# Kernel optimization log

Measured on AMD Instinct MI355X. Metric: run time of the kernel, lower is better.

## Reference

```python
import jax, jax.numpy as jnp
import numpy as np

NUM_HEADS = 16
EPS_LN = 1e-5
EPS_NORM = 1e-12


def layernorm(x, g, b):
    mu = jnp.mean(x, axis=-1, keepdims=True)
    var = jnp.mean((x - mu) ** 2, axis=-1, keepdims=True)
    return (x - mu) * jax.lax.rsqrt(var + EPS_LN) * g + b


def l2norm(x):
    n = jnp.sqrt(jnp.sum(x * x, axis=-1, keepdims=True))
    return x / jnp.maximum(n, EPS_NORM)


def setup_inputs() -> dict:
    key = jax.random.key(0)
    ks = jax.random.split(key, 12)
    B, N, C = 8, 1024, 1024
    std = 0.02
    inp = {
        "txt_token": jax.random.normal(ks[0], (B, 1, C), jnp.float32),
        "text_features": jax.random.normal(ks[1], (B, N, C), jnp.float32),
        "text_mask": jax.random.randint(ks[2], (B, N), 0, 2).astype(bool),
        "vis_token": jax.random.normal(ks[3], (B, 1, C), jnp.float32),
        "top_lens": 256,
        # parameters
        "Wqkv": jax.random.normal(ks[4], (C, 3 * C), jnp.float32) * std,
        "bqkv": jnp.zeros((3 * C,), jnp.float32),
        "Wp2": jax.random.normal(ks[5], (C, C), jnp.float32) * std,
        "bp2": jnp.zeros((C,), jnp.float32),
        "ln2_g": jnp.ones((C,), jnp.float32),
        "ln2_b": jnp.zeros((C,), jnp.float32),
        "sim_alpha": jnp.ones((1,), jnp.float32),
        "sim_beta": jnp.zeros((1,), jnp.float32),
        "Wp1": jax.random.normal(ks[6], (C, C), jnp.float32) * std,
        "bp1": jnp.zeros((C,), jnp.float32),
        "ln1_g": jnp.ones((C,), jnp.float32),
        "ln1_b": jnp.zeros((C,), jnp.float32),
    }
    return inp


def reference(txt_token, text_features, text_mask, vis_token, top_lens,
              Wqkv, bqkv, Wp2, bp2, ln2_g, ln2_b,
              sim_alpha, sim_beta, Wp1, bp1, ln1_g, ln1_b):
    B, N, C = text_features.shape
    H = NUM_HEADS
    hd = C // H
    scale = hd ** (-0.5)

    qkv = (text_features @ Wqkv + bqkv).reshape(B, N, 3, H, hd)
    q = qkv[:, :, 0].transpose(0, 2, 1, 3)  # [B,H,N,hd]
    k = qkv[:, :, 1].transpose(0, 2, 1, 3)
    v = qkv[:, :, 2].transpose(0, 2, 1, 3)

    attn = jnp.einsum('bhqd,bhkd->bhqk', q, k) * scale  # [B,H,N,N]
    vals, idx = jax.lax.top_k(attn, top_lens)            # [B,H,N,k]
    p = jax.nn.softmax(vals, axis=-1)

    # scatter topk softmax back into zeros at original key positions
    b_ix = jnp.arange(B)[:, None, None, None]
    h_ix = jnp.arange(H)[None, :, None, None]
    q_ix = jnp.arange(N)[None, None, :, None]
    attn_sp = jnp.zeros_like(attn).at[b_ix, h_ix, q_ix, idx].set(p)

    # mask padded keys, then second softmax (dropout = identity in eval)
    attn_sp = jnp.where(text_mask[:, None, None, :], -jnp.inf, attn_sp)
    attn_w = jax.nn.softmax(attn_sp, axis=-1)

    x = jnp.einsum('bhqk,bhkd->bqhd', attn_w, v).reshape(B, N, C)
    x = x @ Wp2 + bp2
    tf = layernorm(text_features + x, ln2_g, ln2_b)  # [B,N,C]

    # cosine-similarity top-k pooling
    sim = sim_beta + sim_alpha * jnp.einsum('bmc,bnc->bmn', l2norm(vis_token), l2norm(tf))  # [B,1,N]
    sim = jax.nn.sigmoid(jnp.where(text_mask[:, None, :], -jnp.inf, sim))
    _, top_idx = jax.lax.top_k(sim, top_lens)        # [B,1,k]
    top_idx = top_idx[:, 0]                           # [B,k]
    top_vecs = jnp.take_along_axis(tf, top_idx[:, :, None], axis=1)  # [B,k,C]
    pooled = jnp.mean(top_vecs, axis=1, keepdims=True)               # [B,1,C]

    tt = pooled + txt_token
    tt = layernorm(tt @ Wp1 + bp1, ln1_g, ln1_b)
    return tt, tf
```

## Files before the change

kernel.cpp:

```cpp
#include <hip/hip_runtime.h>
#include <stdint.h>

typedef unsigned short u16;
typedef float floatx4 __attribute__((ext_vector_type(4)));
typedef short short8 __attribute__((ext_vector_type(8)));

#define TOPK_ 256

#define AS1(p) ((const __attribute__((address_space(1))) void*)(p))
#define AS3(p) ((__attribute__((address_space(3))) void*)(p))

__device__ __forceinline__ u16 f2bf(float f) {
  unsigned u = __builtin_bit_cast(unsigned, f);
  unsigned r = (u + 0x7FFFu + ((u >> 16) & 1u)) >> 16;
  return (u16)r;
}
__device__ __forceinline__ float bf2f(u16 b) {
  unsigned u = ((unsigned)b) << 16;
  return __builtin_bit_cast(float, u);
}

__device__ __forceinline__ float wave_sum_f32(float x) {
#define DPP_STEP(ctrl, rmask)                                                        \
  {                                                                                  \
    float t_ = __builtin_bit_cast(                                                   \
        float, __builtin_amdgcn_update_dpp(0, __builtin_bit_cast(int, x), ctrl,      \
                                           rmask, 0xf, true));                       \
    x += t_;                                                                         \
  }
  DPP_STEP(0x111, 0xf)
  DPP_STEP(0x112, 0xf)
  DPP_STEP(0x114, 0xf)
  DPP_STEP(0x118, 0xf)
  DPP_STEP(0x142, 0xa)
  DPP_STEP(0x143, 0xc)
#undef DPP_STEP
  return __builtin_bit_cast(float,
                            __builtin_amdgcn_readlane(__builtin_bit_cast(int, x), 63));
}

__device__ __forceinline__ void wave_sum2_f32(float& x, float& y) {
#define DPP_STEP2(ctrl, rmask)                                                       \
  {                                                                                  \
    float tx_ = __builtin_bit_cast(                                                  \
        float, __builtin_amdgcn_update_dpp(0, __builtin_bit_cast(int, x), ctrl,      \
                                           rmask, 0xf, true));                       \
    float ty_ = __builtin_bit_cast(                                                  \
        float, __builtin_amdgcn_update_dpp(0, __builtin_bit_cast(int, y), ctrl,      \
                                           rmask, 0xf, true));                       \
    x += tx_;                                                                        \
    y += ty_;                                                                        \
  }
  DPP_STEP2(0x111, 0xf)
  DPP_STEP2(0x112, 0xf)
  DPP_STEP2(0x114, 0xf)
  DPP_STEP2(0x118, 0xf)
  DPP_STEP2(0x142, 0xa)
  DPP_STEP2(0x143, 0xc)
#undef DPP_STEP2
  x = __builtin_bit_cast(float, __builtin_amdgcn_readlane(__builtin_bit_cast(int, x), 63));
  y = __builtin_bit_cast(float, __builtin_amdgcn_readlane(__builtin_bit_cast(int, y), 63));
}

__device__ __forceinline__ float block_sum256(float v, volatile float* scratch, int wave,
                                              int lane) {
#pragma unroll
  for (int o = 32; o > 0; o >>= 1) v += __shfl_xor(v, o);
  __syncthreads();
  if (lane == 0) scratch[wave] = v;
  __syncthreads();
  return scratch[0] + scratch[1] + scratch[2] + scratch[3];
}

__global__ __launch_bounds__(256) void prep_kernel(const float* __restrict__ text,
                                                   u16* __restrict__ Abf,
                                                   const float* __restrict__ Wqkv,
                                                   u16* __restrict__ Wtqkv,
                                                   const float* __restrict__ Wp2,
                                                   u16* __restrict__ Wtp2,
                                                   const float* __restrict__ vis,
                                                   float* __restrict__ vhat,
                                                   float* __restrict__ ttpre) {
  __shared__ u16 tile[32][33];
  __shared__ float red[4];
  int blk = blockIdx.x, t = threadIdx.x;
  if (blk < 8192) {
    int i = (blk * 256 + t) * 4;
    float4 v = *reinterpret_cast<const float4*>(text + i);
    ushort4 o;
    o.x = f2bf(v.x); o.y = f2bf(v.y); o.z = f2bf(v.z); o.w = f2bf(v.w);
    *reinterpret_cast<ushort4*>(Abf + i) = o;
  } else if (blk < 12288) {
    const float* W;
    u16* Wt;
    int cols, id;
    if (blk < 11264) { W = Wqkv; Wt = Wtqkv; cols = 3072; id = blk - 8192; }
    else             { W = Wp2;  Wt = Wtp2;  cols = 1024; id = blk - 11264; }
    int nx = cols >> 5;
    int n0 = (id % nx) * 32, k0 = (id / nx) * 32;
    int r = t >> 3, c4 = (t & 7) * 4;
    float4 v = *reinterpret_cast<const float4*>(W + (size_t)(k0 + r) * cols + n0 + c4);
    tile[r][c4 + 0] = f2bf(v.x);
    tile[r][c4 + 1] = f2bf(v.y);
    tile[r][c4 + 2] = f2bf(v.z);
    tile[r][c4 + 3] = f2bf(v.w);
    __syncthreads();
    ushort4 o;
    o.x = tile[c4 + 0][r]; o.y = tile[c4 + 1][r];
    o.z = tile[c4 + 2][r]; o.w = tile[c4 + 3][r];
    *reinterpret_cast<ushort4*>(Wt + (size_t)(n0 + r) * 1024 + k0 + c4) = o;
  } else if (blk < 12296) {
    int b = blk - 12288, wave = t >> 6, lane = t & 63;
    float4 vv = *reinterpret_cast<const float4*>(vis + b * 1024 + t * 4);
    float sq = vv.x * vv.x + vv.y * vv.y + vv.z * vv.z + vv.w * vv.w;
    sq = block_sum256(sq, red, wave, lane);
    float inv = 1.f / fmaxf(sqrtf(sq), 1e-12f);
    float4 o = make_float4(vv.x * inv, vv.y * inv, vv.z * inv, vv.w * inv);
    *reinterpret_cast<float4*>(vhat + b * 1024 + t * 4) = o;
  } else {
    float4 z = make_float4(0.f, 0.f, 0.f, 0.f);
#pragma unroll
    for (int j = 0; j < 8; ++j)
      reinterpret_cast<float4*>(ttpre)[t + j * 256] = z;
  }
}

__global__ __launch_bounds__(256) void gemm_bt(const u16* __restrict__ A,
                                               const u16* __restrict__ Bt,
                                               const float* __restrict__ bias,
                                               int M, int Nn, int K, int mode,
                                               u16* __restrict__ qb, u16* __restrict__ kb,
                                               u16* __restrict__ vb, u16* __restrict__ yb) {
  __shared__ __align__(16) u16 SMEM[32768];
  int id = blockIdx.x + blockIdx.y * gridDim.x;
  int cpx = (gridDim.x * gridDim.y) >> 3;
  int swz = (id & 7) * cpx + (id >> 3);
  int bx = swz % gridDim.x, by = swz / gridDim.x;
  int m0 = by * 128, n0 = bx * 128;
  int t = threadIdx.x, lane = t & 63, wave = t >> 6;
  int wr = wave >> 1, wc = wave & 1;
  int lrow = lane & 15, lko = (lane >> 4) * 8;
  floatx4 acc[4][4];
#pragma unroll
  for (int i = 0; i < 4; ++i)
#pragma unroll
    for (int j = 0; j < 4; ++j) acc[i][j] = (floatx4){0.f, 0.f, 0.f, 0.f};
  int srow = t >> 2, sc8 = (t & 3) * 8;
  const u16* gA0 = A + (size_t)(m0 + srow) * K + sc8;
  const u16* gA1 = A + (size_t)(m0 + srow + 64) * K + sc8;
  const u16* gB0 = Bt + (size_t)(n0 + srow) * K + sc8;
  const u16* gB1 = Bt + (size_t)(n0 + srow + 64) * K + sc8;

#define STAGE_KT(ktv, bufv)                                                              \
  {                                                                                      \
    int koff_ = (ktv) * 32;                                                              \
    u16* dst_ = SMEM + (bufv) * 8192 + t * 8;                                            \
    __builtin_amdgcn_global_load_lds(AS1(gA0 + koff_), AS3(dst_), 16, 0, 0);             \
    __builtin_amdgcn_global_load_lds(AS1(gA1 + koff_), AS3(dst_ + 2048), 16, 0, 0);      \
    __builtin_amdgcn_global_load_lds(AS1(gB0 + koff_), AS3(dst_ + 4096), 16, 0, 0);      \
    __builtin_amdgcn_global_load_lds(AS1(gB1 + koff_), AS3(dst_ + 6144), 16, 0, 0);      \
  }

  STAGE_KT(0, 0)
  STAGE_KT(1, 1)
  const int NKT = 32;
#pragma unroll 1
  for (int kt = 0; kt < NKT; ++kt) {
    int kn = kt + 2;
    if (kn < NKT) STAGE_KT(kn, kn & 3)
    if (kt < NKT - 2)       asm volatile("s_waitcnt vmcnt(8)" ::: "memory");
    else if (kt == NKT - 2) asm volatile("s_waitcnt vmcnt(4)" ::: "memory");
    else                    asm volatile("s_waitcnt vmcnt(0)" ::: "memory");
    __builtin_amdgcn_s_barrier();
    const u16* Asb = SMEM + (kt & 3) * 8192;
    const u16* Bsb = Asb + 4096;
    short8 afr[4], bfr[4];
#pragma unroll
    for (int i = 0; i < 4; ++i) {
      afr[i] = *reinterpret_cast<const short8*>(&Asb[(wr * 64 + i * 16 + lrow) * 32 + lko]);
      bfr[i] = *reinterpret_cast<const short8*>(&Bsb[(wc * 64 + i * 16 + lrow) * 32 + lko]);
    }
#pragma unroll
    for (int i = 0; i < 4; ++i)
#pragma unroll
      for (int j = 0; j < 4; ++j)
        acc[i][j] = __builtin_amdgcn_mfma_f32_16x16x32_bf16(afr[i], bfr[j], acc[i][j], 0, 0, 0);
  }
#undef STAGE_KT

  int rb = (lane >> 4) * 4;
  if (mode == 0 && n0 >= 2048) {
#pragma unroll
    for (int i = 0; i < 4; ++i) {
#pragma unroll
      for (int j = 0; j < 4; ++j) {
        int gcol = n0 + wc * 64 + j * 16 + lrow;
        float bv = bias[gcol];
        int grow0 = m0 + wr * 64 + i * 16 + rb;
        int cc = gcol & 1023, hh = cc >> 6, dd = cc & 63;
        int bb = grow0 >> 10, nq0 = grow0 & 1023;
        size_t headq = ((size_t)bb * 16 + hh);
        int dtile = dd >> 4, drow = dd & 15;
        int ks32 = nq0 >> 5, kk = nq0 & 31, lq = kk >> 3, e = kk & 7;
        int lane2 = lq * 16 + drow;
        ushort4 o;
        o.x = f2bf(acc[i][j][0] + bv);
        o.y = f2bf(acc[i][j][1] + bv);
        o.z = f2bf(acc[i][j][2] + bv);
        o.w = f2bf(acc[i][j][3] + bv);
        *reinterpret_cast<ushort4*>(vb + headq * 65536 + (size_t)ks32 * 2048 +
                                    dtile * 512 + lane2 * 8 + e) = o;
      }
    }
  } else {
    u16* LDSC = SMEM;
    for (int half = 0; half < 2; ++half) {
      __syncthreads();
      if (wc == half) {
#pragma unroll
        for (int i = 0; i < 4; ++i)
#pragma unroll
          for (int j = 0; j < 4; ++j) {
            float bv = bias[n0 + half * 64 + j * 16 + lrow];
#pragma unroll
            for (int rr = 0; rr < 4; ++rr)
              LDSC[(wr * 64 + i * 16 + rb + rr) * 72 + j * 16 + lrow] =
                  f2bf(acc[i][j][rr] + bv);
          }
      }
      __syncthreads();
      int row = t >> 4, c4 = (t & 15) * 4;
#pragma unroll
      for (int it = 0; it < 8; ++it) {
        int rw = row + it * 16;
        ushort4 val = *reinterpret_cast<const ushort4*>(&LDSC[rw * 72 + c4]);
        int grow = m0 + rw, gcol = n0 + half * 64 + c4;
        if (mode == 1) {
          *reinterpret_cast<ushort4*>(yb + (size_t)grow * 1024 + gcol) = val;
        } else {
          int sec = gcol >> 10, cc = gcol & 1023, hh = cc >> 6, dd = cc & 63;
          int bb = grow >> 10, nq = grow & 1023;
          size_t head = ((size_t)bb * 16 + hh);
          if (sec == 0) {
            *reinterpret_cast<ushort4*>(qb + (head * 1024 + nq) * 64 + dd) = val;
          } else {
            int kc = nq >> 4, krow = nq & 15;
            int p = dd >> 5, quad = (dd >> 3) & 3, e = dd & 7;
            *reinterpret_cast<ushort4*>(kb + head * 65536 + (size_t)kc * 1024 +
                                        p * 512 + (quad * 16 + krow) * 8 + e) = val;
          }
        }
      }
    }
  }
}

#define SSTR 1036
__global__ __launch_bounds__(512, 8) void attn_kernel(const u16* __restrict__ qb,
                                                      const u16* __restrict__ kb,
                                                      const u16* __restrict__ vb,
                                                      const int* __restrict__ mask,
                                                      u16* __restrict__ xout) {
  extern __shared__ __align__(16) char smem[];
  u16* Sb = reinterpret_cast<u16*>(smem);
  u16* qs = reinterpret_cast<u16*>(smem + 33152);
  unsigned char* mk8 = reinterpret_cast<unsigned char*>(smem + 35456);
  float* invZs = reinterpret_cast<float*>(smem + 36480);
  float* part = reinterpret_cast<float*>(smem + 36544);

  int blk = blockIdx.x;
  int bh = blk >> 6, qt = blk & 63;
  int b = bh >> 4, h = bh & 15;
  int t = threadIdx.x, wave = t >> 6, lane = t & 63;
  const u16* qh = qb + ((size_t)bh * 1024 + qt * 16) * 64;
  const u16* kh = kb + (size_t)bh * 65536;
  const u16* vh = vb + (size_t)bh * 65536;

  {
    int2 mm = *reinterpret_cast<const int2*>(mask + b * 1024 + t * 2);
    u16 pk = (u16)((mm.x != 0 ? 1u : 0u) | ((mm.y != 0 ? 1u : 0u) << 8));
    *reinterpret_cast<u16*>(&mk8[t * 2]) = pk;
  }
  if (t < 256) {
    int row = t >> 4, c4 = (t & 15) * 4;
    *reinterpret_cast<ushort4*>(&qs[row * 72 + c4]) =
        *reinterpret_cast<const ushort4*>(qh + row * 64 + c4);
  }
  __syncthreads();

  int lrow = lane & 15, lko = (lane >> 4) * 8;
  int quad = lane >> 4;
  int dtile = wave & 3, kq = wave >> 2;
  const u16* vbase = vh + (size_t)(kq * 16 * 4 + dtile) * 512 + lane * 8;

  {
    short8 qf0 = *reinterpret_cast<const short8*>(&qs[lrow * 72 + lko]);
    short8 qf1 = *reinterpret_cast<const short8*>(&qs[lrow * 72 + lko + 32]);
#pragma unroll 4
    for (int c = 0; c < 8; ++c) {
      int kc = wave * 8 + c;
      const u16* kt = kh + (size_t)kc * 1024 + lane * 8;
      short8 kf0 = *reinterpret_cast<const short8*>(kt);
      short8 kf1 = *reinterpret_cast<const short8*>(kt + 512);
      floatx4 acc = (floatx4){0.f, 0.f, 0.f, 0.f};
      acc = __builtin_amdgcn_mfma_f32_16x16x32_bf16(kf0, qf0, acc, 0, 0, 0);
      acc = __builtin_amdgcn_mfma_f32_16x16x32_bf16(kf1, qf1, acc, 0, 0, 0);
      unsigned kk[4];
#pragma unroll
      for (int i = 0; i < 4; ++i) {
        float f = __builtin_fmaf(acc[i], 64.f, 4096.f);
        f = __builtin_amdgcn_fmed3f(f, 0.f, 8191.f);
        kk[i] = (unsigned)f;
      }
      uint2 pk;
      pk.x = __builtin_amdgcn_perm(kk[1], kk[0], 0x05040100u);
      pk.y = __builtin_amdgcn_perm(kk[3], kk[2], 0x05040100u);
      *reinterpret_cast<uint2*>(&Sb[lrow * SSTR + kc * 16 + quad * 4]) = pk;
    }
  }
  __syncthreads();

  short8 vp0 = *reinterpret_cast<const short8*>(vbase);
  short8 vp1 = *reinterpret_cast<const short8*>(vbase + 2048);
  short8 vp2 = *reinterpret_cast<const short8*>(vbase + 4096);
  short8 vp3 = *reinterpret_cast<const short8*>(vbase + 6144);
  asm volatile("" : "+v"(vp0), "+v"(vp1), "+v"(vp2), "+v"(vp3));

  {
    const u16* SrA = Sb + (wave * 2) * SSTR;
    const u16* SrB = Sb + (wave * 2 + 1) * SSTR;
    unsigned kA[16], kB[16];
#pragma unroll
    for (int jj = 0; jj < 4; ++jj) {
      uint2 pa = *reinterpret_cast<const uint2*>(SrA + 4 * lane + 256 * jj);
      uint2 pb = *reinterpret_cast<const uint2*>(SrB + 4 * lane + 256 * jj);
      kA[4 * jj + 0] = pa.x & 0xffffu; kA[4 * jj + 1] = pa.x >> 16;
      kA[4 * jj + 2] = pa.y & 0xffffu; kA[4 * jj + 3] = pa.y >> 16;
      kB[4 * jj + 0] = pb.x & 0xffffu; kB[4 * jj + 1] = pb.x >> 16;
      kB[4 * jj + 2] = pb.y & 0xffffu; kB[4 * jj + 3] = pb.y >> 16;
    }
    unsigned TA = 0, TB = 0;
#pragma unroll
    for (int bit = 12; bit >= 5; --bit) {
      unsigned cA = TA | (1u << bit), cB = TB | (1u << bit);
      int cntA = 0, cntB = 0;
#pragma unroll
      for (int i = 0; i < 16; ++i) {
        cntA += (int)__popcll(__ballot(kA[i] >= cA));
        cntB += (int)__popcll(__ballot(kB[i] >= cB));
      }
      TA = (cntA >= TOPK_) ? cA : TA;
      TB = (cntB >= TOPK_) ? cB : TB;
    }
    unsigned mm[4];
#pragma unroll
    for (int jj = 0; jj < 4; ++jj)
      mm[jj] = *reinterpret_cast<const unsigned*>(mk8 + 4 * lane + 256 * jj);
    const float C1 = 1.44269504f / 512.f;
    const float C0 = -4096.f * (1.44269504f / 512.f);
#pragma unroll 1
    for (int rr = 0; rr < 2; ++rr) {
      int row = wave * 2 + rr;
      unsigned T = rr ? TB : TA;
      unsigned kk[16];
      if (rr == 0) {
#pragma unroll
        for (int i = 0; i < 16; ++i) kk[i] = kA[i];
      } else {
        const u16* Sr = Sb + row * SSTR;
#pragma unroll
        for (int jj = 0; jj < 4; ++jj) {
          uint2 p = *reinterpret_cast<const uint2*>(Sr + 4 * lane + 256 * jj);
          kk[4 * jj + 0] = p.x & 0xffffu; kk[4 * jj + 1] = p.x >> 16;
          kk[4 * jj + 2] = p.y & 0xffffu; kk[4 * jj + 3] = p.y >> 16;
        }
      }
      float e[16];
      float seq[4] = {0.f, 0.f, 0.f, 0.f};
#pragma unroll
      for (int i = 0; i < 16; ++i) {
        float ex = __builtin_amdgcn_exp2f(__builtin_fmaf((float)kk[i], C1, C0));
        ex = (kk[i] >= T) ? ex : 0.f;
        e[i] = ex;
        seq[i & 3] += ex;
      }
      float se = wave_sum_f32((seq[0] + seq[1]) + (seq[2] + seq[3]));
      float cB2 = __builtin_amdgcn_rcpf(se) * 1.44269504f;
      float Z = 0.f;
      u16* Wr = Sb + row * SSTR;
#pragma unroll
      for (int jj = 0; jj < 4; ++jj) {
        unsigned m = mm[jj];
        float w0 = __builtin_amdgcn_exp2f(e[4 * jj + 0] * cB2);
        float w1 = __builtin_amdgcn_exp2f(e[4 * jj + 1] * cB2);
        float w2 = __builtin_amdgcn_exp2f(e[4 * jj + 2] * cB2);
        float w3 = __builtin_amdgcn_exp2f(e[4 * jj + 3] * cB2);
        w0 = (m & 0x000000ffu) ? 0.f : w0;
        w1 = (m & 0x0000ff00u) ? 0.f : w1;
        w2 = (m & 0x00ff0000u) ? 0.f : w2;
        w3 = (m & 0xff000000u) ? 0.f : w3;
        Z += (w0 + w1) + (w2 + w3);
        uint2 pw;
        pw.x = __builtin_amdgcn_perm(__builtin_bit_cast(unsigned, w1),
                                     __builtin_bit_cast(unsigned, w0), 0x07060302u);
        pw.y = __builtin_amdgcn_perm(__builtin_bit_cast(unsigned, w3),
                                     __builtin_bit_cast(unsigned, w2), 0x07060302u);
        *reinterpret_cast<uint2*>(Wr + 4 * lane + 256 * jj) = pw;
      }
      Z = wave_sum_f32(Z);
      if (lane == 0) invZs[row] = __builtin_amdgcn_rcpf(Z);
    }
  }
  __syncthreads();

  {
    floatx4 acc = (floatx4){0.f, 0.f, 0.f, 0.f};
    const u16* wrow = Sb + lrow * SSTR + kq * 512;
    short8 af;
    af = *reinterpret_cast<const short8*>(wrow + 0 * 32 + lko);
    acc = __builtin_amdgcn_mfma_f32_16x16x32_bf16(af, vp0, acc, 0, 0, 0);
    af = *reinterpret_cast<const short8*>(wrow + 1 * 32 + lko);
    acc = __builtin_amdgcn_mfma_f32_16x16x32_bf16(af, vp1, acc, 0, 0, 0);
    af = *reinterpret_cast<const short8*>(wrow + 2 * 32 + lko);
    acc = __builtin_amdgcn_mfma_f32_16x16x32_bf16(af, vp2, acc, 0, 0, 0);
    af = *reinterpret_cast<const short8*>(wrow + 3 * 32 + lko);
    acc = __builtin_amdgcn_mfma_f32_16x16x32_bf16(af, vp3, acc, 0, 0, 0);
#pragma unroll
    for (int ks = 4; ks < 16; ++ks) {
      short8 bf = *reinterpret_cast<const short8*>(vbase + (size_t)ks * 2048);
      short8 af2 = *reinterpret_cast<const short8*>(wrow + ks * 32 + lko);
      acc = __builtin_amdgcn_mfma_f32_16x16x32_bf16(af2, bf, acc, 0, 0, 0);
    }
    if (kq == 1)
      *reinterpret_cast<floatx4*>(part + (size_t)(dtile * 64 + lane) * 4) = acc;
    __syncthreads();
    if (kq == 0) {
      floatx4 p2 = *reinterpret_cast<const floatx4*>(part + (size_t)(dtile * 64 + lane) * 4);
      float4 iz = *reinterpret_cast<const float4*>(&invZs[quad * 4]);
      int d = dtile * 16 + lrow;
      u16* xo = xout + ((size_t)(b * 1024 + qt * 16 + quad * 4)) * 1024 + h * 64 + d;
      xo[0 * 1024] = f2bf((acc[0] + p2[0]) * iz.x);
      xo[1 * 1024] = f2bf((acc[1] + p2[1]) * iz.y);
      xo[2 * 1024] = f2bf((acc[2] + p2[2]) * iz.z);
      xo[3 * 1024] = f2bf((acc[3] + p2[3]) * iz.w);
    }
  }
}

__global__ void resid_ln(const u16* __restrict__ y,
                         const float* __restrict__ text,
                         const float* __restrict__ g,
                         const float* __restrict__ be,
                         const float* __restrict__ vhat,
                         const int* __restrict__ mask,
                         const float* __restrict__ alpha,
                         const float* __restrict__ beta,
                         float* __restrict__ tf,
                         float* __restrict__ sim_g) {
  int wave = threadIdx.x >> 6, lane = threadIdx.x & 63;
  int row = blockIdx.x * 8 + wave;
  int b = row >> 10;
  size_t rbase = (size_t)row * 1024;
  int c0 = lane * 4;
  float v[16];
  float s = 0.f, sq = 0.f;
#pragma unroll
  for (int i = 0; i < 4; ++i) {
    float4 tv = *reinterpret_cast<const float4*>(text + rbase + i * 256 + c0);
    ushort4 yv = *reinterpret_cast<const ushort4*>(y + rbase + i * 256 + c0);
    float a0 = bf2f(yv.x) + tv.x;
    float a1 = bf2f(yv.y) + tv.y;
    float a2 = bf2f(yv.z) + tv.z;
    float a3 = bf2f(yv.w) + tv.w;
    v[i * 4 + 0] = a0; v[i * 4 + 1] = a1; v[i * 4 + 2] = a2; v[i * 4 + 3] = a3;
    s += (a0 + a1) + (a2 + a3);
    sq += (a0 * a0 + a1 * a1) + (a2 * a2 + a3 * a3);
  }
  wave_sum2_f32(s, sq);
  float mean = s * (1.f / 1024.f);
  float var = sq * (1.f / 1024.f) - mean * mean;
  float rs = rsqrtf(var + 1e-5f);
  float s2 = 0.f, dd = 0.f;
#pragma unroll
  for (int i = 0; i < 4; ++i) {
    float4 gv = *reinterpret_cast<const float4*>(g + i * 256 + c0);
    float4 bv = *reinterpret_cast<const float4*>(be + i * 256 + c0);
    float4 hv = *reinterpret_cast<const float4*>(vhat + b * 1024 + i * 256 + c0);
    float o0 = (v[i * 4 + 0] - mean) * rs * gv.x + bv.x;
    float o1 = (v[i * 4 + 1] - mean) * rs * gv.y + bv.y;
    float o2 = (v[i * 4 + 2] - mean) * rs * gv.z + bv.z;
    float o3 = (v[i * 4 + 3] - mean) * rs * gv.w + bv.w;
    float4 ov = make_float4(o0, o1, o2, o3);
    *reinterpret_cast<float4*>(tf + rbase + i * 256 + c0) = ov;
    s2 += (o0 * o0 + o1 * o1) + (o2 * o2 + o3 * o3);
    dd += (o0 * hv.x + o1 * hv.y) + (o2 * hv.z + o3 * hv.w);
  }
  wave_sum2_f32(s2, dd);
  if (lane == 0) {
    float den = fmaxf(sqrtf(s2), 1e-12f);
    float sv = beta[0] + alpha[0] * dd / den;
    sim_g[row] = mask[row] ? -__builtin_inff() : sv;
  }
}

__global__ __launch_bounds__(256) void topk_pool(const float* __restrict__ sim_g,
                                                 const float* __restrict__ tf,
                                                 float* __restrict__ ttpre_acc) {
  __shared__ int idxl[256];
  __shared__ int scount;
  int b = blockIdx.x, p = blockIdx.y, t = threadIdx.x, lane = t & 63;
  if (t == 0) scount = 0;
  __syncthreads();
  if (t < 64) {
    unsigned uv[16];
#pragma unroll
    for (int j = 0; j < 16; ++j) {
      unsigned x = __builtin_bit_cast(unsigned, sim_g[b * 1024 + lane + 64 * j]);
      uv[j] = (x & 0x80000000u) ? ~x : (x | 0x80000000u);
    }
    unsigned T = 0;
    for (int bit = 31; bit >= 0; --bit) {
      unsigned cand = T | (1u << bit);
      int c = 0;
#pragma unroll
      for (int j = 0; j < 16; ++j) c += __popcll(__ballot(uv[j] >= cand));
      if (c >= TOPK_) {
        T = cand;
        if (c == TOPK_) break;
      }
    }
#pragma unroll
    for (int j = 0; j < 16; ++j) {
      if (uv[j] >= T) {
        int q = atomicAdd(&scount, 1);
        if (q < TOPK_) idxl[q] = lane + 64 * j;
      }
    }
  }
  __syncthreads();
  float4 pa = make_float4(0.f, 0.f, 0.f, 0.f);
  for (int i = p * 64; i < p * 64 + 64; ++i) {
    int n = idxl[i];
    float4 vr = *reinterpret_cast<const float4*>(tf + ((size_t)b * 1024 + n) * 1024 + t * 4);
    pa.x += vr.x; pa.y += vr.y; pa.z += vr.z; pa.w += vr.w;
  }
  atomicAdd(&ttpre_acc[b * 1024 + t * 4 + 0], pa.x);
  atomicAdd(&ttpre_acc[b * 1024 + t * 4 + 1], pa.y);
  atomicAdd(&ttpre_acc[b * 1024 + t * 4 + 2], pa.z);
  atomicAdd(&ttpre_acc[b * 1024 + t * 4 + 3], pa.w);
}

__global__ __launch_bounds__(256) void matvec_p1(const float* __restrict__ ttpre_acc,
                                                 const float* __restrict__ txt,
                                                 const float* __restrict__ Wp1,
                                                 const float* __restrict__ bp1,
                                                 float* __restrict__ ttv) {
  __shared__ float xs[1024];
  __shared__ float red[4][64];
  int b = blockIdx.x, q = blockIdx.y, t = threadIdx.x;
  for (int j = t; j < 1024; j += 256)
    xs[j] = ttpre_acc[b * 1024 + j] * (1.f / 256.f) + txt[b * 1024 + j];
  __syncthreads();
  int r = t >> 6, col = q * 64 + (t & 63);
  float acc = 0.f;
#pragma unroll 8
  for (int c = r * 256; c < r * 256 + 256; ++c) acc += xs[c] * Wp1[(size_t)c * 1024 + col];
  red[r][t & 63] = acc;
  __syncthreads();
  if (t < 64) {
    float o = red[0][t] + red[1][t] + red[2][t] + red[3][t] + bp1[q * 64 + t];
    ttv[b * 1024 + q * 64 + t] = o;
  }
}

__global__ __launch_bounds__(256) void ln_tt(const float* __restrict__ ttv,
                                             const float* __restrict__ g1,
                                             const float* __restrict__ b1,
                                             float* __restrict__ tt_out) {
  __shared__ float red[4];
  int b = blockIdx.x, t = threadIdx.x, wave = t >> 6, lane = t & 63;
  float4 v = *reinterpret_cast<const float4*>(ttv + b * 1024 + t * 4);
  float s = v.x + v.y + v.z + v.w;
  float sq = v.x * v.x + v.y * v.y + v.z * v.z + v.w * v.w;
  s = block_sum256(s, red, wave, lane);
  sq = block_sum256(sq, red, wave, lane);
  float mean = s * (1.f / 1024.f);
  float var = sq * (1.f / 1024.f) - mean * mean;
  float rs = rsqrtf(var + 1e-5f);
  float4 gv = *reinterpret_cast<const float4*>(g1 + t * 4);
  float4 bv = *reinterpret_cast<const float4*>(b1 + t * 4);
  float4 o;
  o.x = (v.x - mean) * rs * gv.x + bv.x;
  o.y = (v.y - mean) * rs * gv.y + bv.y;
  o.z = (v.z - mean) * rs * gv.z + bv.z;
  o.w = (v.w - mean) * rs * gv.w + bv.w;
  *reinterpret_cast<float4*>(tt_out + b * 1024 + t * 4) = o;
}

extern "C" void kernel_launch(void* const* d_in, const int* in_sizes, int n_in, void* d_out,
                              int out_size, void* d_ws, size_t ws_size, hipStream_t stream) {
  (void)in_sizes; (void)n_in; (void)out_size; (void)ws_size;
  const float* txt = (const float*)d_in[0];
  const float* text = (const float*)d_in[1];
  const int* mask = (const int*)d_in[2];
  const float* vis = (const float*)d_in[3];
  const float* Wqkv = (const float*)d_in[5];
  const float* bqkv = (const float*)d_in[6];
  const float* Wp2 = (const float*)d_in[7];
  const float* bp2 = (const float*)d_in[8];
  const float* g2 = (const float*)d_in[9];
  const float* b2 = (const float*)d_in[10];
  const float* alpha = (const float*)d_in[11];
  const float* beta = (const float*)d_in[12];
  const float* Wp1 = (const float*)d_in[13];
  const float* bp1 = (const float*)d_in[14];
  const float* g1 = (const float*)d_in[15];
  const float* b1 = (const float*)d_in[16];

  char* ws = (char*)d_ws;
  const size_t MB = 1u << 20;
  u16* Abf = (u16*)(ws);
  u16* Wtqkv = (u16*)(ws + 16 * MB);
  u16* Wtp2 = (u16*)(ws + 22 * MB);
  u16* qbuf = (u16*)(ws + 24 * MB);
  u16* kbuf = (u16*)(ws + 40 * MB);
  u16* vbuf = (u16*)(ws + 56 * MB);
  u16* ybuf = (u16*)(ws + 72 * MB);
  float* vhat = (float*)(ws + 88 * MB);
  float* sim_g = (float*)(ws + 88 * MB + 65536);
  float* ttpre = (float*)(ws + 88 * MB + 131072);
  float* ttv = (float*)(ws + 88 * MB + 196608);

  float* out = (float*)d_out;
  float* tt_out = out;
  float* tf_out = out + 8 * 1024;

  prep_kernel<<<dim3(12297), dim3(256), 0, stream>>>(text, Abf, Wqkv, Wtqkv, Wp2, Wtp2, vis,
                                                     vhat, ttpre);
  gemm_bt<<<dim3(24, 64), dim3(256), 0, stream>>>(Abf, Wtqkv, bqkv, 8192, 3072, 1024, 0, qbuf,
                                                  kbuf, vbuf, (u16*)nullptr);
  attn_kernel<<<dim3(8192), dim3(512), 40640, stream>>>(qbuf, kbuf, vbuf, mask, Abf);
  gemm_bt<<<dim3(8, 64), dim3(256), 0, stream>>>(Abf, Wtp2, bp2, 8192, 1024, 1024, 1,
                                                 (u16*)nullptr, (u16*)nullptr, (u16*)nullptr,
                                                 ybuf);
  resid_ln<<<dim3(1024), dim3(512), 0, stream>>>(ybuf, text, g2, b2, vhat, mask, alpha, beta,
                                                 tf_out, sim_g);
  topk_pool<<<dim3(8, 4), dim3(256), 0, stream>>>(sim_g, tf_out, ttpre);
  matvec_p1<<<dim3(8, 16), dim3(256), 0, stream>>>(ttpre, txt, Wp1, bp1, ttv);
  ln_tt<<<dim3(8), dim3(256), 0, stream>>>(ttv, g1, b1, tt_out);
}
```

Before: 425.9 us.

## Pre-swizzle weights into MFMA fragment layout and load B directly to registers

The weight transpose kernel now writes Wt in a tiled layout that matches the MFMA 16x16x32 B-fragment lane ordering. The GEMM loads B fragments straight from global memory into registers, double-buffered across k-steps, instead of staging them through LDS. This halves shared memory use and removes the B-side LDS traffic. In exchange, global load latency is exposed on the register path and more registers are used, which may lower occupancy.

Result: no change. 426.4 us (+0.1%).

```diff
diff --git a/kernel.cpp b/kernel.cpp
--- a/kernel.cpp
+++ b/kernel.cpp
@@ -108,7 +108,13 @@
     ushort4 o;
     o.x = tile[c4 + 0][r]; o.y = tile[c4 + 1][r];
     o.z = tile[c4 + 2][r]; o.w = tile[c4 + 3][r];
-    *reinterpret_cast<ushort4*>(Wt + (size_t)(n0 + r) * 1024 + k0 + c4) = o;
+    int n = n0 + r;
+    int ntile = n >> 4, nr = n & 15;
+    int kt = k0 >> 5;
+    int lq = (c4 & 31) >> 3;
+    int e0 = c4 & 7;
+    size_t addr = (((size_t)ntile * 32 + kt) * 64 + (lq * 16 + nr)) * 8 + e0;
+    *reinterpret_cast<ushort4*>(Wt + addr) = o;
   } else if (blk < 12296) {
     int b = blk - 12288, wave = t >> 6, lane = t & 63;
     float4 vv = *reinterpret_cast<const float4*>(vis + b * 1024 + t * 4);
@@ -131,7 +137,7 @@
                                                int M, int Nn, int K, int mode,
                                                u16* __restrict__ qb, u16* __restrict__ kb,
                                                u16* __restrict__ vb, u16* __restrict__ yb) {
-  __shared__ __align__(16) u16 SMEM[32768];
+  __shared__ __align__(16) u16 SMEM[16384];
   int id = blockIdx.x + blockIdx.y * gridDim.x;
   int cpx = (gridDim.x * gridDim.y) >> 3;
   int swz = (id & 7) * cpx + (id >> 3);
@@ -148,44 +154,52 @@
   int srow = t >> 2, sc8 = (t & 3) * 8;
   const u16* gA0 = A + (size_t)(m0 + srow) * K + sc8;
   const u16* gA1 = A + (size_t)(m0 + srow + 64) * K + sc8;
-  const u16* gB0 = Bt + (size_t)(n0 + srow) * K + sc8;
-  const u16* gB1 = Bt + (size_t)(n0 + srow + 64) * K + sc8;
-
-#define STAGE_KT(ktv, bufv)                                                              \
+  const u16* Bw = Bt + ((size_t)(bx * 8 + wc * 4) * 32) * 512 + lane * 8;
+
+#define STAGE_KT(ktv)                                                                    \
   {                                                                                      \
     int koff_ = (ktv) * 32;                                                              \
-    u16* dst_ = SMEM + (bufv) * 8192 + t * 8;                                            \
+    u16* dst_ = SMEM + ((ktv) & 3) * 4096 + t * 8;                                       \
     __builtin_amdgcn_global_load_lds(AS1(gA0 + koff_), AS3(dst_), 16, 0, 0);             \
     __builtin_amdgcn_global_load_lds(AS1(gA1 + koff_), AS3(dst_ + 2048), 16, 0, 0);      \
-    __builtin_amdgcn_global_load_lds(AS1(gB0 + koff_), AS3(dst_ + 4096), 16, 0, 0);      \
-    __builtin_amdgcn_global_load_lds(AS1(gB1 + koff_), AS3(dst_ + 6144), 16, 0, 0);      \
-  }
-
-  STAGE_KT(0, 0)
-  STAGE_KT(1, 1)
-  const int NKT = 32;
+  }
+#define LOADB(dstv, ktv)                                                                 \
+  {                                                                                      \
+    dstv[0] = *reinterpret_cast<const short8*>(Bw + (size_t)(0 * 32 + (ktv)) * 512);     \
+    dstv[1] = *reinterpret_cast<const short8*>(Bw + (size_t)(1 * 32 + (ktv)) * 512);     \
+    dstv[2] = *reinterpret_cast<const short8*>(Bw + (size_t)(2 * 32 + (ktv)) * 512);     \
+    dstv[3] = *reinterpret_cast<const short8*>(Bw + (size_t)(3 * 32 + (ktv)) * 512);     \
+  }
+#define GBODY(ktv, BCUR, BNEXT)                                                          \
+  {                                                                                      \
+    if ((ktv) + 2 < 32) STAGE_KT((ktv) + 2)                                              \
+    if ((ktv) + 1 < 32) LOADB(BNEXT, (ktv) + 1)                                          \
+    if ((ktv) <= 29)      asm volatile("s_waitcnt vmcnt(6)" ::: "memory");               \
+    else if ((ktv) == 30) asm volatile("s_waitcnt vmcnt(4)" ::: "memory");               \
+    else                  asm volatile("s_waitcnt vmcnt(0)" ::: "memory");               \
+    __builtin_amdgcn_s_barrier();                                                        \
+    const u16* Asb = SMEM + ((ktv) & 3) * 4096;                                          \
+    short8 afr[4];                                                                       \
+    _Pragma("unroll") for (int i_ = 0; i_ < 4; ++i_)                                     \
+        afr[i_] = *reinterpret_cast<const short8*>(                                      \
+            &Asb[(wr * 64 + i_ * 16 + lrow) * 32 + lko]);                                \
+    _Pragma("unroll") for (int i_ = 0; i_ < 4; ++i_)                                     \
+        _Pragma("unroll") for (int j_ = 0; j_ < 4; ++j_)                                 \
+            acc[i_][j_] = __builtin_amdgcn_mfma_f32_16x16x32_bf16(afr[i_], BCUR[j_],     \
+                                                                  acc[i_][j_], 0, 0, 0); \
+  }
+
+  short8 b0[4], b1[4];
+  STAGE_KT(0)
+  STAGE_KT(1)
+  LOADB(b0, 0)
 #pragma unroll 1
-  for (int kt = 0; kt < NKT; ++kt) {
-    int kn = kt + 2;
-    if (kn < NKT) STAGE_KT(kn, kn & 3)
-    if (kt < NKT - 2)       asm volatile("s_waitcnt vmcnt(8)" ::: "memory");
-    else if (kt == NKT - 2) asm volatile("s_waitcnt vmcnt(4)" ::: "memory");
-    else                    asm volatile("s_waitcnt vmcnt(0)" ::: "memory");
-    __builtin_amdgcn_s_barrier();
-    const u16* Asb = SMEM + (kt & 3) * 8192;
-    const u16* Bsb = Asb + 4096;
-    short8 afr[4], bfr[4];
-#pragma unroll
-    for (int i = 0; i < 4; ++i) {
-      afr[i] = *reinterpret_cast<const short8*>(&Asb[(wr * 64 + i * 16 + lrow) * 32 + lko]);
-      bfr[i] = *reinterpret_cast<const short8*>(&Bsb[(wc * 64 + i * 16 + lrow) * 32 + lko]);
-    }
-#pragma unroll
-    for (int i = 0; i < 4; ++i)
-#pragma unroll
-      for (int j = 0; j < 4; ++j)
-        acc[i][j] = __builtin_amdgcn_mfma_f32_16x16x32_bf16(afr[i], bfr[j], acc[i][j], 0, 0, 0);
-  }
+  for (int kt = 0; kt < 32; kt += 2) {
+    GBODY(kt, b0, b1)
+    GBODY(kt + 1, b1, b0)
+  }
+#undef GBODY
+#undef LOADB
 #undef STAGE_KT
 
   int rb = (lane >> 4) * 4;
```
